# Kernel tuning notes

Measured on AMD Instinct MI355X. Metric: run time of the kernel, lower is better.

The kernel has to match this reference:

```python
import jax, jax.numpy as jnp
import numpy as np

N_NODES, N_GRAPHS, HIDDEN, N_BRANCH = 131072, 4096, 512, 4
G_HEAD, N_HEAD = 50, 3  # graph head dim, node head dim; var_output=1 doubles MLP output


def setup_inputs() -> dict:
    key = jax.random.key(0)
    ks = jax.random.split(key, 10)
    s = 0.02
    x = jax.random.normal(ks[0], (N_NODES, HIDDEN), dtype=jnp.float32)
    # sorted graph assignment: 32 nodes per graph (consecutive, as unique_consecutive assumes)
    batch = (jnp.arange(N_NODES) // (N_NODES // N_GRAPHS)).astype(jnp.int32)
    dataset_ids = jax.random.randint(ks[1], (N_GRAPHS,), 0, N_BRANCH).astype(jnp.int32)
    return {
        "x": x,
        "Ws": jax.random.normal(ks[2], (N_BRANCH, HIDDEN, HIDDEN)) * s,
        "bs": jnp.zeros((N_BRANCH, HIDDEN)),
        "Wg": jax.random.normal(ks[3], (N_BRANCH, HIDDEN, 2 * G_HEAD)) * s,
        "bg": jnp.zeros((N_BRANCH, 2 * G_HEAD)),
        "Wn1": jax.random.normal(ks[4], (N_BRANCH, HIDDEN, HIDDEN)) * s,
        "bn1": jnp.zeros((N_BRANCH, HIDDEN)),
        "Wn2": jax.random.normal(ks[5], (N_BRANCH, HIDDEN, 2 * N_HEAD)) * s,
        "bn2": jnp.zeros((N_BRANCH, 2 * N_HEAD)),
        "batch": batch,
        "dataset_ids": dataset_ids,
    }


def reference(x, Ws, bs, Wg, bg, Wn1, bn1, Wn2, bn2, batch, dataset_ids):
    n_graphs = dataset_ids.shape[0]
    n_branch = Ws.shape[0]
    ghd = Wg.shape[2] // 2
    nhd = Wn2.shape[2] // 2
    # mean pooling per graph (graph_pool_fn with 'mean' reduction)
    ones = jnp.ones((x.shape[0],), dtype=x.dtype)
    counts = jax.ops.segment_sum(ones, batch, num_segments=n_graphs)
    x_graph = jax.ops.segment_sum(x, batch, num_segments=n_graphs) / counts[:, None]
    node_ds = dataset_ids[batch]  # per-node branch id (repeat_interleave of graph mask)

    g_head = jnp.zeros((n_graphs, ghd), dtype=x.dtype)
    g_var = jnp.zeros((n_graphs, ghd), dtype=x.dtype)
    n_head_out = jnp.zeros((x.shape[0], nhd), dtype=x.dtype)
    n_var = jnp.zeros((x.shape[0], nhd), dtype=x.dtype)
    for b in range(n_branch):  # fixed small branch set (structurally distinct experts)
        # graph head branch: graph_shared MLP -> head MLP, scatter back via mask
        hg = jax.nn.relu(x_graph @ Ws[b] + bs[b])
        og = hg @ Wg[b] + bg[b]
        mg = (dataset_ids == b).astype(x.dtype)[:, None]
        g_head = g_head + mg * og[:, :ghd]
        g_var = g_var + mg * (og[:, ghd:] ** 2)
        # node head branch (node_NN_type == 'mlp')
        hn = jax.nn.relu(x @ Wn1[b] + bn1[b])
        on = hn @ Wn2[b] + bn2[b]
        mn = (node_ds == b).astype(x.dtype)[:, None]
        n_head_out = n_head_out + mn * on[:, :nhd]
        n_var = n_var + mn * (on[:, nhd:] ** 2)
    return (g_head, g_var, n_head_out, n_var)
```

## Files before the change

### kernel.cpp

```cpp
#include <hip/hip_runtime.h>

#define N_NODES  131072
#define N_GRAPHS 4096
#define HID      512

typedef float  f32x4  __attribute__((ext_vector_type(4)));
typedef __bf16 bf16x8 __attribute__((ext_vector_type(8)));
typedef unsigned short u16x8 __attribute__((ext_vector_type(8)));

__device__ __forceinline__ unsigned short f2bf(float f) {
  unsigned int u = __builtin_bit_cast(unsigned int, f);
  u += 0x7FFFu + ((u >> 16) & 1u);
  return (unsigned short)(u >> 16);
}
__device__ __forceinline__ f32x4 mfma_bf16(bf16x8 a, bf16x8 b, f32x4 c) {
  return __builtin_amdgcn_mfma_f32_16x16x32_bf16(a, b, c, 0, 0, 0);
}

__global__ __launch_bounds__(256) void bucket_kernel(
    const int* __restrict__ dsid, int* __restrict__ perm, int* __restrict__ meta) {
  __shared__ int cnt[4], base[4], off[4];
  int t = threadIdx.x;
  if (t < 4) { cnt[t] = 0; off[t] = 0; }
  __syncthreads();
  for (int g = t; g < N_GRAPHS; g += 256) atomicAdd(&cnt[dsid[g]], 1);
  __syncthreads();
  if (t == 0) {
    int s = 0;
    for (int b = 0; b < 4; ++b) { base[b] = s; s += cnt[b]; meta[b] = cnt[b]; }
  }
  __syncthreads();
  for (int g = t; g < N_GRAPHS; g += 256) {
    int b = dsid[g];
    int p = base[b] + atomicAdd(&off[b], 1);
    perm[p] = g;
  }
}

__global__ __launch_bounds__(256) void prep_wf_kernel(
    const float* __restrict__ Wn1, const float* __restrict__ Ws,
    unsigned short* __restrict__ W1Tf, unsigned short* __restrict__ WsTf) {
  __shared__ unsigned short lt[8192];
  const int bid = blockIdx.x;
  const int which = bid >> 7;
  const int b  = (bid >> 5) & 3;
  const int hf = bid & 31;
  const float* src = (which ? Ws : Wn1) + (size_t)b * 512 * 512 + hf * 16;
  unsigned short* dst = (which ? WsTf : W1Tf) + (size_t)(b * 32 + hf) * 8192;
  const int t = threadIdx.x;
  for (int i = t; i < 8192; i += 256) {
    int k = i >> 4;
    int n = i & 15;
    float v = src[(size_t)k * 512 + n];
    int kk = k >> 5, lane = n + ((k >> 3) & 3) * 16, e = k & 7;
    lt[(kk * 64 + lane) * 8 + e] = f2bf(v);
  }
  __syncthreads();
  u16x8* d8 = (u16x8*)dst;
  const u16x8* s8 = (const u16x8*)lt;
  for (int i = t; i < 1024; i += 256) d8[i] = s8[i];
}

__global__ __launch_bounds__(256) void prep_wg_kernel(
    const float* __restrict__ Wg, unsigned short* __restrict__ WgT) {
  int idx = blockIdx.x * 256 + threadIdx.x;
  int b = idx >> 16;
  int r = (idx >> 9) & 127;
  int k = idx & 511;
  float v = (r < 100) ? Wg[(b * 512 + k) * 100 + r] : 0.f;
  WgT[idx] = f2bf(v);
}

#define NT_MAX 2050
__global__ __launch_bounds__(1024, 2) void node_kernel(
    const float* __restrict__ x,
    const int* __restrict__ meta,
    const int* __restrict__ perm,
    const unsigned short* __restrict__ W1Tf,
    const float* __restrict__ bn1,
    const float* __restrict__ Wn2,
    const float* __restrict__ bn2,
    unsigned short* __restrict__ xg,
    float* __restrict__ n_head,
    float* __restrict__ n_var) {
  __shared__ __align__(16) unsigned short xfrag[2][8192];
  __shared__ __align__(16) float psum[2][16][128];

  const int4 cvv = *(const int4*)meta;
  const int cnts[4] = {cvv.x, cvv.y, cvv.z, cvv.w};
  int i = blockIdx.x, branch = -1, permOff = 0, nvalid = 0, pb = 0;
  for (int b = 0; b < 4; ++b) {
    int nt = (cnts[b] + 1) >> 1;
    if (branch < 0 && i < nt) { branch = b; permOff = pb + i * 2; nvalid = min(2, cnts[b] - i * 2); }
    if (branch < 0) i -= nt;
    pb += cnts[b];
  }
  if (branch < 0) return;

  const int t    = threadIdx.x;
  const int lane = t & 63;
  const int w    = t >> 6;
  const int l15  = lane & 15;
  const int l4   = lane >> 4;

  const int g0 = perm[permOff];
  const int g1 = perm[permOff + (nvalid > 1 ? 1 : 0)];

  const int sr = t >> 4;
  const int so = t & 15;
  const float* srcbase = x + ((size_t)(sr >= 32 ? g1 : g0) * 32 + (sr & 31)) * HID + so * 8;
  const int sn = sr >> 4, sl15 = sr & 15, skkl = so >> 2, sl4 = so & 3;
  const int welem = ((sn * 4 + skkl) * 64 + ((sl4 << 4) | (sl15 ^ so))) * 8;

  const unsigned short* wb0 = W1Tf + (size_t)(branch * 32 + w * 2) * 8192 + lane * 8;

  f32x4 acc[2][4];
  #pragma unroll
  for (int m = 0; m < 2; ++m)
    #pragma unroll
    for (int n = 0; n < 4; ++n) acc[m][n] = (f32x4)0.f;

  float4 p0 = *(const float4*)(srcbase);
  float4 p1 = *(const float4*)(srcbase + 4);

  #pragma unroll
  for (int c = 0; c < 4; ++c) {
    u16x8 ua;
    ua[0]=f2bf(p0.x); ua[1]=f2bf(p0.y); ua[2]=f2bf(p0.z); ua[3]=f2bf(p0.w);
    ua[4]=f2bf(p1.x); ua[5]=f2bf(p1.y); ua[6]=f2bf(p1.z); ua[7]=f2bf(p1.w);
    *(u16x8*)&xfrag[c & 1][welem] = ua;

    float s[8];
    s[0]=p0.x; s[1]=p0.y; s[2]=p0.z; s[3]=p0.w;
    s[4]=p1.x; s[5]=p1.y; s[6]=p1.z; s[7]=p1.w;
    #pragma unroll
    for (int j = 0; j < 8; ++j) {
      s[j] += __shfl_xor(s[j], 16);
      s[j] += __shfl_xor(s[j], 32);
    }
    if (lane < 16) {
      f32x4 a4; a4[0]=s[0]; a4[1]=s[1]; a4[2]=s[2]; a4[3]=s[3];
      f32x4 b4; b4[0]=s[4]; b4[1]=s[5]; b4[2]=s[6]; b4[3]=s[7];
      *(f32x4*)&psum[c & 1][w][lane * 8]     = a4;
      *(f32x4*)&psum[c & 1][w][lane * 8 + 4] = b4;
    }

    if (c < 3) {
      p0 = *(const float4*)(srcbase + (c + 1) * 128);
      p1 = *(const float4*)(srcbase + (c + 1) * 128 + 4);
    }
    __syncthreads();

    if (t < 256) {
      int gg = t >> 7, cc = t & 127;
      if (gg == 0 || nvalid > 1) {
        float sv = 0.f;
        #pragma unroll
        for (int j = 0; j < 8; ++j) sv += psum[c & 1][gg * 8 + j][cc];
        xg[(size_t)(gg ? g1 : g0) * HID + c * 128 + cc] = f2bf(sv * (1.f / 32.f));
      }
    }

    __builtin_amdgcn_s_setprio(1);
    #pragma unroll
    for (int kk = 0; kk < 4; ++kk) {
      bf16x8 af0 = *(const bf16x8*)(wb0 + (size_t)(c * 4 + kk) * 512);
      bf16x8 af1 = *(const bf16x8*)(wb0 + 8192 + (size_t)(c * 4 + kk) * 512);
      const int rslot = (l4 << 4) | (l15 ^ (kk * 4 + l4));
      bf16x8 bfr[4];
      #pragma unroll
      for (int n = 0; n < 4; ++n)
        bfr[n] = *(const bf16x8*)&xfrag[c & 1][((n * 4 + kk) * 64 + rslot) * 8];
      #pragma unroll
      for (int n = 0; n < 4; ++n) {
        acc[0][n] = mfma_bf16(af0, bfr[n], acc[0][n]);
        acc[1][n] = mfma_bf16(af1, bfr[n], acc[1][n]);
      }
    }
    __builtin_amdgcn_s_setprio(0);
  }

  __syncthreads();

  float part[4][6];
  #pragma unroll
  for (int n = 0; n < 4; ++n)
    #pragma unroll
    for (int j = 0; j < 6; ++j) part[n][j] = 0.f;
  const float* W2 = Wn2 + branch * HID * 6;
  const float* B1 = bn1 + branch * HID;
  #pragma unroll
  for (int m = 0; m < 2; ++m) {
    #pragma unroll
    for (int r = 0; r < 4; ++r) {
      int hcol = w * 32 + m * 16 + l4 * 4 + r;
      float b1 = B1[hcol];
      float w2[6];
      #pragma unroll
      for (int j = 0; j < 6; ++j) w2[j] = W2[hcol * 6 + j];
      #pragma unroll
      for (int n = 0; n < 4; ++n) {
        float h = fmaxf(acc[m][n][r] + b1, 0.f);
        #pragma unroll
        for (int j = 0; j < 6; ++j) part[n][j] += h * w2[j];
      }
    }
  }
  #pragma unroll
  for (int n = 0; n < 4; ++n)
    #pragma unroll
    for (int j = 0; j < 6; ++j) {
      part[n][j] += __shfl_xor(part[n][j], 16);
      part[n][j] += __shfl_xor(part[n][j], 32);
    }
  float (*red)[17][7] = (float (*)[17][7])&xfrag[0][0];
  if (lane < 16) {
    #pragma unroll
    for (int n = 0; n < 4; ++n)
      #pragma unroll
      for (int j = 0; j < 6; ++j) red[n * 16 + l15][w][j] = part[n][j];
  }
  __syncthreads();
  if (t < 64) {
    int row = t;
    if (row < nvalid * 32) {
      int node = (row < 32 ? g0 : g1) * 32 + (row & 31);
      #pragma unroll
      for (int j = 0; j < 6; ++j) {
        float sv = bn2[branch * 6 + j];
        #pragma unroll
        for (int ww = 0; ww < 16; ++ww) sv += red[row][ww][j];
        if (j < 3) n_head[(size_t)node * 3 + j] = sv;
        else       n_var[(size_t)node * 3 + (j - 3)] = sv * sv;
      }
    }
  }
}

#define GT_MAX 67
__global__ __launch_bounds__(512, 4) void gstage1_kernel(
    const unsigned short* __restrict__ xg,
    const int* __restrict__ meta,
    const int* __restrict__ perm,
    const unsigned short* __restrict__ WsTf,
    const float* __restrict__ bs_,
    unsigned short* __restrict__ hg) {
  __shared__ __align__(16) unsigned short xtile[4 * 16 * 512];
  __shared__ int gidl[64];

  const int4 cv = *(const int4*)meta;
  const int cnts[4] = {cv.x, cv.y, cv.z, cv.w};

  int i = blockIdx.x, branch = -1, permOff = 0, nvalid = 0, pb = 0;
  for (int b = 0; b < 4; ++b) {
    int gt = (cnts[b] + 63) >> 6;
    if (branch < 0 && i < gt) { branch = b; permOff = pb + i * 64; nvalid = min(64, cnts[b] - i * 64); }
    if (branch < 0) i -= gt;
    pb += cnts[b];
  }
  if (branch < 0) return;

  const int t    = threadIdx.x;
  const int lane = t & 63;
  const int w    = t >> 6;
  const int l15  = lane & 15;
  const int l4   = lane >> 4;

  if (t < 64) gidl[t] = perm[permOff + min(t, nvalid - 1)];
  __syncthreads();

  for (int idx = t; idx < 4096; idx += 512) {
    int row = idx >> 6;
    int c8  = (idx & 63) * 8;
    u16x8 v = *(const u16x8*)&xg[(size_t)gidl[row] * HID + c8];
    int kk = c8 >> 5, ln = (c8 >> 3) & 3;
    *(u16x8*)&xtile[(((row >> 4) * 16 + kk) * 64 + ((row & 15) + ln * 16)) * 8] = v;
  }
  __syncthreads();

  f32x4 acc[4][4];
  #pragma unroll
  for (int m = 0; m < 4; ++m)
    #pragma unroll
    for (int n = 0; n < 4; ++n) acc[m][n] = (f32x4)0.f;

  const unsigned short* wbase = WsTf + ((size_t)(branch * 32 + w * 4)) * 8192 + lane * 8;
  const unsigned short* xbase = xtile + lane * 8;
  #pragma unroll
  for (int kk = 0; kk < 16; ++kk) {
    bf16x8 af[4];
    #pragma unroll
    for (int m = 0; m < 4; ++m)
      af[m] = *(const bf16x8*)(wbase + (m * 16 + kk) * 512);
    bf16x8 bfr[4];
    #pragma unroll
    for (int n = 0; n < 4; ++n)
      bfr[n] = *(const bf16x8*)(xbase + (n * 16 + kk) * 512);
    #pragma unroll
    for (int m = 0; m < 4; ++m)
      #pragma unroll
      for (int n = 0; n < 4; ++n)
        acc[m][n] = mfma_bf16(af[m], bfr[n], acc[m][n]);
  }

  const float* B1 = bs_ + branch * HID;
  #pragma unroll
  for (int m = 0; m < 4; ++m) {
    #pragma unroll
    for (int n = 0; n < 4; ++n) {
      int row = n * 16 + l15;
      if (row < nvalid) {
        int g = gidl[row];
        int hcb = w * 64 + m * 16 + l4 * 4;
        ushort4 hv;
        hv.x = f2bf(fmaxf(acc[m][n][0] + B1[hcb + 0], 0.f));
        hv.y = f2bf(fmaxf(acc[m][n][1] + B1[hcb + 1], 0.f));
        hv.z = f2bf(fmaxf(acc[m][n][2] + B1[hcb + 2], 0.f));
        hv.w = f2bf(fmaxf(acc[m][n][3] + B1[hcb + 3], 0.f));
        *(ushort4*)(hg + (size_t)g * HID + hcb) = hv;
      }
    }
  }
}

#define G2_MAX 259
__global__ __launch_bounds__(256) void gstage2_kernel(
    const int* __restrict__ meta,
    const int* __restrict__ perm,
    const unsigned short* __restrict__ hg,
    const unsigned short* __restrict__ WgT,
    const float* __restrict__ bg,
    float* __restrict__ g_head,
    float* __restrict__ g_var) {
  __shared__ int gidl[16];
  const int4 cv = *(const int4*)meta;
  const int cnts[4] = {cv.x, cv.y, cv.z, cv.w};

  int i = blockIdx.x, branch = -1, permOff = 0, nvalid = 0, pb = 0;
  for (int b = 0; b < 4; ++b) {
    int gt = (cnts[b] + 15) >> 4;
    if (branch < 0 && i < gt) { branch = b; permOff = pb + i * 16; nvalid = min(16, cnts[b] - i * 16); }
    if (branch < 0) i -= gt;
    pb += cnts[b];
  }
  if (branch < 0) return;

  const int t    = threadIdx.x;
  const int lane = t & 63;
  const int w    = t >> 6;
  const int l15  = lane & 15;
  const int l4   = lane >> 4;

  if (t < 16) gidl[t] = perm[permOff + min(t, nvalid - 1)];
  __syncthreads();

  f32x4 acc2[2];
  acc2[0] = (f32x4)0.f; acc2[1] = (f32x4)0.f;
  const unsigned short* arow = hg + (size_t)gidl[l15] * HID + l4 * 8;
  const unsigned short* brow = WgT + ((size_t)branch * 128 + w * 32 + l15) * 512 + l4 * 8;
  #pragma unroll
  for (int ks = 0; ks < 16; ++ks) {
    bf16x8 a  = *(const bf16x8*)(arow + ks * 32);
    bf16x8 b0 = *(const bf16x8*)(brow + ks * 32);
    bf16x8 b1 = *(const bf16x8*)(brow + 16 * 512 + ks * 32);
    acc2[0] = mfma_bf16(a, b0, acc2[0]);
    acc2[1] = mfma_bf16(a, b1, acc2[1]);
  }
  #pragma unroll
  for (int n2 = 0; n2 < 2; ++n2) {
    int j = w * 32 + n2 * 16 + l15;
    if (j < 100) {
      float bias = bg[branch * 100 + j];
      #pragma unroll
      for (int rr = 0; rr < 4; ++rr) {
        int r = l4 * 4 + rr;
        if (r < nvalid) {
          int g = gidl[r];
          float val = acc2[n2][rr] + bias;
          if (j < 50) g_head[(size_t)g * 50 + j] = val;
          else        g_var[(size_t)g * 50 + (j - 50)] = val * val;
        }
      }
    }
  }
}

extern "C" void kernel_launch(void* const* d_in, const int* in_sizes, int n_in,
                              void* d_out, int out_size, void* d_ws, size_t ws_size,
                              hipStream_t stream) {
  const float* x    = (const float*)d_in[0];
  const float* Ws   = (const float*)d_in[1];
  const float* bs   = (const float*)d_in[2];
  const float* Wg   = (const float*)d_in[3];
  const float* bg   = (const float*)d_in[4];
  const float* Wn1  = (const float*)d_in[5];
  const float* bn1  = (const float*)d_in[6];
  const float* Wn2  = (const float*)d_in[7];
  const float* bn2  = (const float*)d_in[8];
  const int* dsid   = (const int*)d_in[10];

  float* out    = (float*)d_out;
  float* g_head = out;
  float* g_var  = out + (size_t)N_GRAPHS * 50;
  float* n_head = out + (size_t)2 * N_GRAPHS * 50;
  float* n_var  = n_head + (size_t)N_NODES * 3;

  char* ws = (char*)d_ws;
  int* perm = (int*)(ws);
  int* meta = (int*)(ws + 16384);
  unsigned short* W1Tf = (unsigned short*)(ws + 16640);
  unsigned short* WsTf = (unsigned short*)(ws + 2113792);
  unsigned short* WgT  = (unsigned short*)(ws + 4210944);
  unsigned short* xg   = (unsigned short*)(ws + 4735232);
  unsigned short* hg   = (unsigned short*)(ws + 8929536);
  if (ws_size < 13123840) return;

  bucket_kernel<<<dim3(1), dim3(256), 0, stream>>>(dsid, perm, meta);
  prep_wf_kernel<<<dim3(256), dim3(256), 0, stream>>>(Wn1, Ws, W1Tf, WsTf);
  prep_wg_kernel<<<dim3(1024), dim3(256), 0, stream>>>(Wg, WgT);
  node_kernel<<<dim3(NT_MAX), dim3(1024), 0, stream>>>(
      x, meta, perm, W1Tf, bn1, Wn2, bn2, xg, n_head, n_var);
  gstage1_kernel<<<dim3(GT_MAX), dim3(512), 0, stream>>>(
      xg, meta, perm, WsTf, bs, hg);
  gstage2_kernel<<<dim3(G2_MAX), dim3(256), 0, stream>>>(
      meta, perm, hg, WgT, bg, g_head, g_var);
}
```

Measured before the change: 220.6 us.

## Restructure node kernel to one graph per 256-thread block

The node MLP kernel now processes one graph (32 nodes) per 256-thread block, reading the branch directly from dataset_ids instead of the bucketed permutation. Each wave covers 128 hidden columns over 8 K-chunks, which gives more MFMA work per B fragment and a smaller shared-memory footprint so more blocks fit per CU. Each block now streams the full branch weight matrix for only 32 nodes instead of 64, which doubles the weight traffic from L2 relative to node data. The mean-pool reduction is deferred until after the matmul loop.

```diff
diff --git a/kernel.cpp b/kernel.cpp
--- a/kernel.cpp
+++ b/kernel.cpp
@@ -71,11 +71,9 @@
   WgT[idx] = f2bf(v);
 }
 
-#define NT_MAX 2050
-__global__ __launch_bounds__(1024, 2) void node_kernel(
+__global__ __launch_bounds__(256, 4) void node_kernel(
     const float* __restrict__ x,
-    const int* __restrict__ meta,
-    const int* __restrict__ perm,
+    const int* __restrict__ dsid,
     const unsigned short* __restrict__ W1Tf,
     const float* __restrict__ bn1,
     const float* __restrict__ Wn2,
@@ -83,48 +81,35 @@
     unsigned short* __restrict__ xg,
     float* __restrict__ n_head,
     float* __restrict__ n_var) {
-  __shared__ __align__(16) unsigned short xfrag[2][8192];
-  __shared__ __align__(16) float psum[2][16][128];
-
-  const int4 cvv = *(const int4*)meta;
-  const int cnts[4] = {cvv.x, cvv.y, cvv.z, cvv.w};
-  int i = blockIdx.x, branch = -1, permOff = 0, nvalid = 0, pb = 0;
-  for (int b = 0; b < 4; ++b) {
-    int nt = (cnts[b] + 1) >> 1;
-    if (branch < 0 && i < nt) { branch = b; permOff = pb + i * 2; nvalid = min(2, cnts[b] - i * 2); }
-    if (branch < 0) i -= nt;
-    pb += cnts[b];
-  }
-  if (branch < 0) return;
-
+  __shared__ __align__(16) unsigned short xfrag[2][2048];
+  __shared__ __align__(16) float psum[8][4][64];
+  __shared__ __align__(16) float red[4][32][6];
+
+  const int g = blockIdx.x;
+  const int b = dsid[g];
   const int t    = threadIdx.x;
   const int lane = t & 63;
   const int w    = t >> 6;
   const int l15  = lane & 15;
   const int l4   = lane >> 4;
 
-  const int g0 = perm[permOff];
-  const int g1 = perm[permOff + (nvalid > 1 ? 1 : 0)];
-
-  const int sr = t >> 4;
-  const int so = t & 15;
-  const float* srcbase = x + ((size_t)(sr >= 32 ? g1 : g0) * 32 + (sr & 31)) * HID + so * 8;
-  const int sn = sr >> 4, sl15 = sr & 15, skkl = so >> 2, sl4 = so & 3;
-  const int welem = ((sn * 4 + skkl) * 64 + ((sl4 << 4) | (sl15 ^ so))) * 8;
-
-  const unsigned short* wb0 = W1Tf + (size_t)(branch * 32 + w * 2) * 8192 + lane * 8;
-
-  f32x4 acc[2][4];
-  #pragma unroll
-  for (int m = 0; m < 2; ++m)
-    #pragma unroll
-    for (int n = 0; n < 4; ++n) acc[m][n] = (f32x4)0.f;
-
-  float4 p0 = *(const float4*)(srcbase);
-  float4 p1 = *(const float4*)(srcbase + 4);
-
-  #pragma unroll
-  for (int c = 0; c < 4; ++c) {
+  const int srow = t >> 3;
+  const int oct  = t & 7;
+  const float* src = x + ((size_t)g * 32 + srow) * HID + oct * 8;
+  const int sn = srow >> 4, skk = oct >> 2, sl4 = oct & 3;
+  const int welem = ((sn * 2 + skk) * 64 + ((sl4 << 4) | ((srow & 15) ^ oct))) * 8;
+
+  const unsigned short* wb = W1Tf + (size_t)(b * 32 + w * 8) * 8192 + lane * 8;
+
+  f32x4 acc[8][2];
+  #pragma unroll
+  for (int m = 0; m < 8; ++m) { acc[m][0] = (f32x4)0.f; acc[m][1] = (f32x4)0.f; }
+
+  float4 p0 = *(const float4*)(src);
+  float4 p1 = *(const float4*)(src + 4);
+
+  #pragma unroll
+  for (int c = 0; c < 8; ++c) {
     u16x8 ua;
     ua[0]=f2bf(p0.x); ua[1]=f2bf(p0.y); ua[2]=f2bf(p0.z); ua[3]=f2bf(p0.w);
     ua[4]=f2bf(p1.x); ua[5]=f2bf(p1.y); ua[6]=f2bf(p1.z); ua[7]=f2bf(p1.w);
@@ -135,71 +120,66 @@
     s[4]=p1.x; s[5]=p1.y; s[6]=p1.z; s[7]=p1.w;
     #pragma unroll
     for (int j = 0; j < 8; ++j) {
+      s[j] += __shfl_xor(s[j], 8);
       s[j] += __shfl_xor(s[j], 16);
       s[j] += __shfl_xor(s[j], 32);
     }
-    if (lane < 16) {
+    if (lane < 8) {
       f32x4 a4; a4[0]=s[0]; a4[1]=s[1]; a4[2]=s[2]; a4[3]=s[3];
       f32x4 b4; b4[0]=s[4]; b4[1]=s[5]; b4[2]=s[6]; b4[3]=s[7];
-      *(f32x4*)&psum[c & 1][w][lane * 8]     = a4;
-      *(f32x4*)&psum[c & 1][w][lane * 8 + 4] = b4;
-    }
-
-    if (c < 3) {
-      p0 = *(const float4*)(srcbase + (c + 1) * 128);
-      p1 = *(const float4*)(srcbase + (c + 1) * 128 + 4);
+      *(f32x4*)&psum[c][w][lane * 8]     = a4;
+      *(f32x4*)&psum[c][w][lane * 8 + 4] = b4;
+    }
+
+    if (c < 7) {
+      p0 = *(const float4*)(src + (c + 1) * 64);
+      p1 = *(const float4*)(src + (c + 1) * 64 + 4);
     }
     __syncthreads();
 
-    if (t < 256) {
-      int gg = t >> 7, cc = t & 127;
-      if (gg == 0 || nvalid > 1) {
-        float sv = 0.f;
-        #pragma unroll
-        for (int j = 0; j < 8; ++j) sv += psum[c & 1][gg * 8 + j][cc];
-        xg[(size_t)(gg ? g1 : g0) * HID + c * 128 + cc] = f2bf(sv * (1.f / 32.f));
+    __builtin_amdgcn_s_setprio(1);
+    #pragma unroll
+    for (int kk = 0; kk < 2; ++kk) {
+      const int kkG = c * 2 + kk;
+      const int rslot = (l4 << 4) | (l15 ^ (kk * 4 + l4));
+      bf16x8 bfr0 = *(const bf16x8*)&xfrag[c & 1][((kk) * 64 + rslot) * 8];
+      bf16x8 bfr1 = *(const bf16x8*)&xfrag[c & 1][((2 + kk) * 64 + rslot) * 8];
+      #pragma unroll
+      for (int m = 0; m < 8; ++m) {
+        bf16x8 af = *(const bf16x8*)(wb + (size_t)m * 8192 + kkG * 512);
+        acc[m][0] = mfma_bf16(af, bfr0, acc[m][0]);
+        acc[m][1] = mfma_bf16(af, bfr1, acc[m][1]);
       }
     }
-
-    __builtin_amdgcn_s_setprio(1);
-    #pragma unroll
-    for (int kk = 0; kk < 4; ++kk) {
-      bf16x8 af0 = *(const bf16x8*)(wb0 + (size_t)(c * 4 + kk) * 512);
-      bf16x8 af1 = *(const bf16x8*)(wb0 + 8192 + (size_t)(c * 4 + kk) * 512);
-      const int rslot = (l4 << 4) | (l15 ^ (kk * 4 + l4));
-      bf16x8 bfr[4];
-      #pragma unroll
-      for (int n = 0; n < 4; ++n)
-        bfr[n] = *(const bf16x8*)&xfrag[c & 1][((n * 4 + kk) * 64 + rslot) * 8];
-      #pragma unroll
-      for (int n = 0; n < 4; ++n) {
-        acc[0][n] = mfma_bf16(af0, bfr[n], acc[0][n]);
-        acc[1][n] = mfma_bf16(af1, bfr[n], acc[1][n]);
-      }
-    }
     __builtin_amdgcn_s_setprio(0);
   }
 
-  __syncthreads();
-
-  float part[4][6];
-  #pragma unroll
-  for (int n = 0; n < 4; ++n)
+  #pragma unroll
+  for (int h = 0; h < 2; ++h) {
+    int col = t + h * 256;
+    int c = col >> 6, cc = col & 63;
+    float sv = psum[c][0][cc] + psum[c][1][cc] + psum[c][2][cc] + psum[c][3][cc];
+    xg[(size_t)g * HID + col] = f2bf(sv * (1.f / 32.f));
+  }
+
+  float part[2][6];
+  #pragma unroll
+  for (int n = 0; n < 2; ++n)
     #pragma unroll
     for (int j = 0; j < 6; ++j) part[n][j] = 0.f;
-  const float* W2 = Wn2 + branch * HID * 6;
-  const float* B1 = bn1 + branch * HID;
-  #pragma unroll
-  for (int m = 0; m < 2; ++m) {
+  const float* W2 = Wn2 + b * HID * 6;
+  const float* B1 = bn1 + b * HID;
+  #pragma unroll
+  for (int m = 0; m < 8; ++m) {
     #pragma unroll
     for (int r = 0; r < 4; ++r) {
-      int hcol = w * 32 + m * 16 + l4 * 4 + r;
+      int hcol = w * 128 + m * 16 + l4 * 4 + r;
       float b1 = B1[hcol];
       float w2[6];
       #pragma unroll
       for (int j = 0; j < 6; ++j) w2[j] = W2[hcol * 6 + j];
       #pragma unroll
-      for (int n = 0; n < 4; ++n) {
+      for (int n = 0; n < 2; ++n) {
         float h = fmaxf(acc[m][n][r] + b1, 0.f);
         #pragma unroll
         for (int j = 0; j < 6; ++j) part[n][j] += h * w2[j];
@@ -207,32 +187,28 @@
     }
   }
   #pragma unroll
-  for (int n = 0; n < 4; ++n)
+  for (int n = 0; n < 2; ++n)
     #pragma unroll
     for (int j = 0; j < 6; ++j) {
       part[n][j] += __shfl_xor(part[n][j], 16);
       part[n][j] += __shfl_xor(part[n][j], 32);
     }
-  float (*red)[17][7] = (float (*)[17][7])&xfrag[0][0];
   if (lane < 16) {
     #pragma unroll
-    for (int n = 0; n < 4; ++n)
-      #pragma unroll
-      for (int j = 0; j < 6; ++j) red[n * 16 + l15][w][j] = part[n][j];
-  }
-  __syncthreads();
-  if (t < 64) {
+    for (int n = 0; n < 2; ++n)
+      #pragma unroll
+      for (int j = 0; j < 6; ++j) red[w][n * 16 + l15][j] = part[n][j];
+  }
+  __syncthreads();
+  if (t < 32) {
     int row = t;
-    if (row < nvalid * 32) {
-      int node = (row < 32 ? g0 : g1) * 32 + (row & 31);
-      #pragma unroll
-      for (int j = 0; j < 6; ++j) {
-        float sv = bn2[branch * 6 + j];
-        #pragma unroll
-        for (int ww = 0; ww < 16; ++ww) sv += red[row][ww][j];
-        if (j < 3) n_head[(size_t)node * 3 + j] = sv;
-        else       n_var[(size_t)node * 3 + (j - 3)] = sv * sv;
-      }
+    int node = g * 32 + row;
+    #pragma unroll
+    for (int j = 0; j < 6; ++j) {
+      float sv = red[0][row][j] + red[1][row][j] + red[2][row][j] + red[3][row][j]
+               + bn2[b * 6 + j];
+      if (j < 3) n_head[(size_t)node * 3 + j] = sv;
+      else       n_var[(size_t)node * 3 + (j - 3)] = sv * sv;
     }
   }
 }
@@ -418,8 +394,8 @@
   bucket_kernel<<<dim3(1), dim3(256), 0, stream>>>(dsid, perm, meta);
   prep_wf_kernel<<<dim3(256), dim3(256), 0, stream>>>(Wn1, Ws, W1Tf, WsTf);
   prep_wg_kernel<<<dim3(1024), dim3(256), 0, stream>>>(Wg, WgT);
-  node_kernel<<<dim3(NT_MAX), dim3(1024), 0, stream>>>(
-      x, meta, perm, W1Tf, bn1, Wn2, bn2, xg, n_head, n_var);
+  node_kernel<<<dim3(N_GRAPHS), dim3(256), 0, stream>>>(
+      x, dsid, W1Tf, bn1, Wn2, bn2, xg, n_head, n_var);
   gstage1_kernel<<<dim3(GT_MAX), dim3(512), 0, stream>>>(
       xg, meta, perm, WsTf, bs, hg);
   gstage2_kernel<<<dim3(G2_MAX), dim3(256), 0, stream>>>(
```

New measurement: 393.4 us. +78.4%, slower.

## Split node stage into chunked bf16 convert/pool and GEMM kernels

Applied to the files above, without the earlier changes.

The fused node kernel is replaced by a per-chunk pair of kernels. A convert_pool kernel writes x as bf16 MFMA-fragment tiles plus pooled graph means, and a node_gemm kernel with 512 threads loads two graphs' full tiles into shared memory and runs the whole K loop from LDS. Graph bucketing is now done per 1024-graph chunk so each GEMM launch only touches data converted for its chunk, which should keep it L2-resident. This adds a large bf16 workspace round trip, 8 launches instead of 1, and extra partially filled blocks in the graph stages.

```diff
diff --git a/kernel.cpp b/kernel.cpp
--- a/kernel.cpp
+++ b/kernel.cpp
@@ -3,6 +3,9 @@
 #define N_NODES  131072
 #define N_GRAPHS 4096
 #define HID      512
+#define CHUNK_G  1024
+#define N_CHUNKS 4
+#define B_BLOCKS 516
 
 typedef float  f32x4  __attribute__((ext_vector_type(4)));
 typedef __bf16 bf16x8 __attribute__((ext_vector_type(8)));
@@ -17,23 +20,22 @@
   return __builtin_amdgcn_mfma_f32_16x16x32_bf16(a, b, c, 0, 0, 0);
 }
 
-__global__ __launch_bounds__(256) void bucket_kernel(
+__global__ __launch_bounds__(512) void bucket_kernel(
     const int* __restrict__ dsid, int* __restrict__ perm, int* __restrict__ meta) {
-  __shared__ int cnt[4], base[4], off[4];
+  __shared__ int cnt[N_CHUNKS][4], base[N_CHUNKS][4], off[N_CHUNKS][4];
   int t = threadIdx.x;
-  if (t < 4) { cnt[t] = 0; off[t] = 0; }
-  __syncthreads();
-  for (int g = t; g < N_GRAPHS; g += 256) atomicAdd(&cnt[dsid[g]], 1);
-  __syncthreads();
-  if (t == 0) {
+  if (t < N_CHUNKS * 4) { (&cnt[0][0])[t] = 0; (&off[0][0])[t] = 0; }
+  __syncthreads();
+  for (int g = t; g < N_GRAPHS; g += 512) atomicAdd(&cnt[g / CHUNK_G][dsid[g]], 1);
+  __syncthreads();
+  if (t < N_CHUNKS) {
     int s = 0;
-    for (int b = 0; b < 4; ++b) { base[b] = s; s += cnt[b]; meta[b] = cnt[b]; }
-  }
-  __syncthreads();
-  for (int g = t; g < N_GRAPHS; g += 256) {
-    int b = dsid[g];
-    int p = base[b] + atomicAdd(&off[b], 1);
-    perm[p] = g;
+    for (int b = 0; b < 4; ++b) { base[t][b] = s; s += cnt[t][b]; meta[t * 4 + b] = cnt[t][b]; }
+  }
+  __syncthreads();
+  for (int g = t; g < N_GRAPHS; g += 512) {
+    int c = g / CHUNK_G, b = dsid[g];
+    perm[c * CHUNK_G + base[c][b] + atomicAdd(&off[c][b], 1)] = g;
   }
 }
 
@@ -71,22 +73,71 @@
   WgT[idx] = f2bf(v);
 }
 
-#define NT_MAX 2050
-__global__ __launch_bounds__(1024, 2) void node_kernel(
+__global__ __launch_bounds__(512) void convert_pool_kernel(
     const float* __restrict__ x,
-    const int* __restrict__ meta,
-    const int* __restrict__ perm,
+    unsigned short* __restrict__ xb,
+    unsigned short* __restrict__ xg,
+    int gbase) {
+  const int gl = blockIdx.x;
+  const int g  = gbase + gl;
+  const int t = threadIdx.x;
+  const int lane = t & 63, w = t >> 6, l15 = lane & 15, l4 = lane >> 4;
+  const float* xs = x + (size_t)g * 32 * HID;
+  unsigned short* xd = xb + (size_t)gl * 16384;
+  float ps[2][8];
+  #pragma unroll
+  for (int j = 0; j < 2; ++j)
+    #pragma unroll
+    for (int e = 0; e < 8; ++e) ps[j][e] = 0.f;
+  #pragma unroll
+  for (int i = 0; i < 4; ++i) {
+    const int kk = w * 2 + (i & 1), nf = i >> 1, pi = i & 1;
+    const int row = nf * 16 + l15, col = kk * 32 + l4 * 8;
+    float4 p0 = *(const float4*)(xs + (size_t)row * HID + col);
+    float4 p1 = *(const float4*)(xs + (size_t)row * HID + col + 4);
+    u16x8 ua;
+    ua[0]=f2bf(p0.x); ua[1]=f2bf(p0.y); ua[2]=f2bf(p0.z); ua[3]=f2bf(p0.w);
+    ua[4]=f2bf(p1.x); ua[5]=f2bf(p1.y); ua[6]=f2bf(p1.z); ua[7]=f2bf(p1.w);
+    *(u16x8*)&xd[((nf * 16 + kk) * 64 + lane) * 8] = ua;
+    ps[pi][0]+=p0.x; ps[pi][1]+=p0.y; ps[pi][2]+=p0.z; ps[pi][3]+=p0.w;
+    ps[pi][4]+=p1.x; ps[pi][5]+=p1.y; ps[pi][6]+=p1.z; ps[pi][7]+=p1.w;
+  }
+  #pragma unroll
+  for (int j = 0; j < 2; ++j)
+    #pragma unroll
+    for (int e = 0; e < 8; ++e) {
+      ps[j][e] += __shfl_xor(ps[j][e], 1);
+      ps[j][e] += __shfl_xor(ps[j][e], 2);
+      ps[j][e] += __shfl_xor(ps[j][e], 4);
+      ps[j][e] += __shfl_xor(ps[j][e], 8);
+    }
+  if (l15 == 0) {
+    #pragma unroll
+    for (int j = 0; j < 2; ++j) {
+      int kk = w * 2 + j;
+      u16x8 o;
+      #pragma unroll
+      for (int e = 0; e < 8; ++e) o[e] = f2bf(ps[j][e] * (1.f / 32.f));
+      *(u16x8*)&xg[(size_t)g * HID + kk * 32 + l4 * 8] = o;
+    }
+  }
+}
+
+__global__ __launch_bounds__(512, 4) void node_gemm_kernel(
+    const unsigned short* __restrict__ xb,
+    const int* __restrict__ metac,
+    const int* __restrict__ permc,
     const unsigned short* __restrict__ W1Tf,
     const float* __restrict__ bn1,
     const float* __restrict__ Wn2,
     const float* __restrict__ bn2,
-    unsigned short* __restrict__ xg,
     float* __restrict__ n_head,
-    float* __restrict__ n_var) {
-  __shared__ __align__(16) unsigned short xfrag[2][8192];
-  __shared__ __align__(16) float psum[2][16][128];
-
-  const int4 cvv = *(const int4*)meta;
+    float* __restrict__ n_var,
+    int gbase) {
+  __shared__ __align__(16) unsigned short xtile[32768];
+  __shared__ __align__(16) float red[8][64][6];
+
+  const int4 cvv = *(const int4*)metac;
   const int cnts[4] = {cvv.x, cvv.y, cvv.z, cvv.w};
   int i = blockIdx.x, branch = -1, permOff = 0, nvalid = 0, pb = 0;
   for (int b = 0; b < 4; ++b) {
@@ -97,115 +148,72 @@
   }
   if (branch < 0) return;
 
-  const int t    = threadIdx.x;
-  const int lane = t & 63;
-  const int w    = t >> 6;
-  const int l15  = lane & 15;
-  const int l4   = lane >> 4;
-
-  const int g0 = perm[permOff];
-  const int g1 = perm[permOff + (nvalid > 1 ? 1 : 0)];
-
-  const int sr = t >> 4;
-  const int so = t & 15;
-  const float* srcbase = x + ((size_t)(sr >= 32 ? g1 : g0) * 32 + (sr & 31)) * HID + so * 8;
-  const int sn = sr >> 4, sl15 = sr & 15, skkl = so >> 2, sl4 = so & 3;
-  const int welem = ((sn * 4 + skkl) * 64 + ((sl4 << 4) | (sl15 ^ so))) * 8;
-
-  const unsigned short* wb0 = W1Tf + (size_t)(branch * 32 + w * 2) * 8192 + lane * 8;
-
-  f32x4 acc[2][4];
-  #pragma unroll
-  for (int m = 0; m < 2; ++m)
-    #pragma unroll
-    for (int n = 0; n < 4; ++n) acc[m][n] = (f32x4)0.f;
-
-  float4 p0 = *(const float4*)(srcbase);
-  float4 p1 = *(const float4*)(srcbase + 4);
-
-  #pragma unroll
-  for (int c = 0; c < 4; ++c) {
-    u16x8 ua;
-    ua[0]=f2bf(p0.x); ua[1]=f2bf(p0.y); ua[2]=f2bf(p0.z); ua[3]=f2bf(p0.w);
-    ua[4]=f2bf(p1.x); ua[5]=f2bf(p1.y); ua[6]=f2bf(p1.z); ua[7]=f2bf(p1.w);
-    *(u16x8*)&xfrag[c & 1][welem] = ua;
-
-    float s[8];
-    s[0]=p0.x; s[1]=p0.y; s[2]=p0.z; s[3]=p0.w;
-    s[4]=p1.x; s[5]=p1.y; s[6]=p1.z; s[7]=p1.w;
-    #pragma unroll
-    for (int j = 0; j < 8; ++j) {
-      s[j] += __shfl_xor(s[j], 16);
-      s[j] += __shfl_xor(s[j], 32);
-    }
-    if (lane < 16) {
-      f32x4 a4; a4[0]=s[0]; a4[1]=s[1]; a4[2]=s[2]; a4[3]=s[3];
-      f32x4 b4; b4[0]=s[4]; b4[1]=s[5]; b4[2]=s[6]; b4[3]=s[7];
-      *(f32x4*)&psum[c & 1][w][lane * 8]     = a4;
-      *(f32x4*)&psum[c & 1][w][lane * 8 + 4] = b4;
-    }
-
-    if (c < 3) {
-      p0 = *(const float4*)(srcbase + (c + 1) * 128);
-      p1 = *(const float4*)(srcbase + (c + 1) * 128 + 4);
-    }
-    __syncthreads();
-
-    if (t < 256) {
-      int gg = t >> 7, cc = t & 127;
-      if (gg == 0 || nvalid > 1) {
-        float sv = 0.f;
-        #pragma unroll
-        for (int j = 0; j < 8; ++j) sv += psum[c & 1][gg * 8 + j][cc];
-        xg[(size_t)(gg ? g1 : g0) * HID + c * 128 + cc] = f2bf(sv * (1.f / 32.f));
-      }
-    }
-
-    __builtin_amdgcn_s_setprio(1);
-    #pragma unroll
-    for (int kk = 0; kk < 4; ++kk) {
-      bf16x8 af0 = *(const bf16x8*)(wb0 + (size_t)(c * 4 + kk) * 512);
-      bf16x8 af1 = *(const bf16x8*)(wb0 + 8192 + (size_t)(c * 4 + kk) * 512);
-      const int rslot = (l4 << 4) | (l15 ^ (kk * 4 + l4));
+  const int t = threadIdx.x;
+  const int lane = t & 63, w = t >> 6, l15 = lane & 15, l4 = lane >> 4;
+  const int g0 = permc[permOff];
+  const int g1 = permc[permOff + (nvalid > 1 ? 1 : 0)];
+
+  const unsigned short* s0 = xb + (size_t)(g0 - gbase) * 16384;
+  const unsigned short* s1 = xb + (size_t)(g1 - gbase) * 16384;
+  #pragma unroll
+  for (int ii = 0; ii < 4; ++ii) {
+    int idx = (t + ii * 512) * 8;
+    *(u16x8*)&xtile[idx]         = *(const u16x8*)&s0[idx];
+    *(u16x8*)&xtile[16384 + idx] = *(const u16x8*)&s1[idx];
+  }
+  __syncthreads();
+
+  float part[4][6];
+  #pragma unroll
+  for (int n = 0; n < 4; ++n)
+    #pragma unroll
+    for (int j = 0; j < 6; ++j) part[n][j] = 0.f;
+  const float* B1 = bn1 + branch * HID;
+  const float* W2 = Wn2 + branch * HID * 6;
+
+  #pragma unroll
+  for (int s = 0; s < 2; ++s) {
+    const unsigned short* wb =
+        W1Tf + ((size_t)(branch * 32 + s * 16 + w * 2)) * 8192 + lane * 8;
+    f32x4 acc[2][4];
+    #pragma unroll
+    for (int m = 0; m < 2; ++m)
+      #pragma unroll
+      for (int n = 0; n < 4; ++n) acc[m][n] = (f32x4)0.f;
+
+    #pragma unroll
+    for (int kk = 0; kk < 16; ++kk) {
+      bf16x8 af0 = *(const bf16x8*)(wb + kk * 512);
+      bf16x8 af1 = *(const bf16x8*)(wb + 8192 + kk * 512);
       bf16x8 bfr[4];
       #pragma unroll
       for (int n = 0; n < 4; ++n)
-        bfr[n] = *(const bf16x8*)&xfrag[c & 1][((n * 4 + kk) * 64 + rslot) * 8];
+        bfr[n] = *(const bf16x8*)&xtile[(n * 16 + kk) * 512 + lane * 8];
       #pragma unroll
       for (int n = 0; n < 4; ++n) {
         acc[0][n] = mfma_bf16(af0, bfr[n], acc[0][n]);
         acc[1][n] = mfma_bf16(af1, bfr[n], acc[1][n]);
       }
     }
-    __builtin_amdgcn_s_setprio(0);
-  }
-
-  __syncthreads();
-
-  float part[4][6];
-  #pragma unroll
-  for (int n = 0; n < 4; ++n)
-    #pragma unroll
-    for (int j = 0; j < 6; ++j) part[n][j] = 0.f;
-  const float* W2 = Wn2 + branch * HID * 6;
-  const float* B1 = bn1 + branch * HID;
-  #pragma unroll
-  for (int m = 0; m < 2; ++m) {
-    #pragma unroll
-    for (int r = 0; r < 4; ++r) {
-      int hcol = w * 32 + m * 16 + l4 * 4 + r;
-      float b1 = B1[hcol];
-      float w2[6];
-      #pragma unroll
-      for (int j = 0; j < 6; ++j) w2[j] = W2[hcol * 6 + j];
-      #pragma unroll
-      for (int n = 0; n < 4; ++n) {
-        float h = fmaxf(acc[m][n][r] + b1, 0.f);
+    #pragma unroll
+    for (int m = 0; m < 2; ++m) {
+      #pragma unroll
+      for (int r = 0; r < 4; ++r) {
+        int hcol = (s * 16 + w * 2 + m) * 16 + l4 * 4 + r;
+        float b1 = B1[hcol];
+        float w2[6];
         #pragma unroll
-        for (int j = 0; j < 6; ++j) part[n][j] += h * w2[j];
+        for (int j = 0; j < 6; ++j) w2[j] = W2[hcol * 6 + j];
+        #pragma unroll
+        for (int n = 0; n < 4; ++n) {
+          float h = fmaxf(acc[m][n][r] + b1, 0.f);
+          #pragma unroll
+          for (int j = 0; j < 6; ++j) part[n][j] += h * w2[j];
+        }
       }
     }
   }
+
   #pragma unroll
   for (int n = 0; n < 4; ++n)
     #pragma unroll
@@ -213,23 +221,22 @@
       part[n][j] += __shfl_xor(part[n][j], 16);
       part[n][j] += __shfl_xor(part[n][j], 32);
     }
-  float (*red)[17][7] = (float (*)[17][7])&xfrag[0][0];
   if (lane < 16) {
     #pragma unroll
     for (int n = 0; n < 4; ++n)
       #pragma unroll
-      for (int j = 0; j < 6; ++j) red[n * 16 + l15][w][j] = part[n][j];
+      for (int j = 0; j < 6; ++j) red[w][n * 16 + l15][j] = part[n][j];
   }
   __syncthreads();
   if (t < 64) {
-    int row = t;
-    if (row < nvalid * 32) {
-      int node = (row < 32 ? g0 : g1) * 32 + (row & 31);
+    int q = t >> 5;
+    if (q < nvalid) {
+      int node = (q ? g1 : g0) * 32 + (t & 31);
       #pragma unroll
       for (int j = 0; j < 6; ++j) {
         float sv = bn2[branch * 6 + j];
         #pragma unroll
-        for (int ww = 0; ww < 16; ++ww) sv += red[row][ww][j];
+        for (int ww = 0; ww < 8; ++ww) sv += red[ww][t][j];
         if (j < 3) n_head[(size_t)node * 3 + j] = sv;
         else       n_var[(size_t)node * 3 + (j - 3)] = sv * sv;
       }
@@ -237,7 +244,7 @@
   }
 }
 
-#define GT_MAX 67
+#define GT_MAX 80
 __global__ __launch_bounds__(512, 4) void gstage1_kernel(
     const unsigned short* __restrict__ xg,
     const int* __restrict__ meta,
@@ -245,26 +252,24 @@
     const unsigned short* __restrict__ WsTf,
     const float* __restrict__ bs_,
     unsigned short* __restrict__ hg) {
-  __shared__ __align__(16) unsigned short xtile[4 * 16 * 512];
+  __shared__ __align__(16) unsigned short xtile[32768];
   __shared__ int gidl[64];
 
-  const int4 cv = *(const int4*)meta;
-  const int cnts[4] = {cv.x, cv.y, cv.z, cv.w};
-
-  int i = blockIdx.x, branch = -1, permOff = 0, nvalid = 0, pb = 0;
-  for (int b = 0; b < 4; ++b) {
-    int gt = (cnts[b] + 63) >> 6;
-    if (branch < 0 && i < gt) { branch = b; permOff = pb + i * 64; nvalid = min(64, cnts[b] - i * 64); }
-    if (branch < 0) i -= gt;
-    pb += cnts[b];
+  int i = blockIdx.x, branch = -1, permOff = 0, nvalid = 0;
+  for (int c = 0; c < N_CHUNKS; ++c) {
+    int pb = 0;
+    for (int b = 0; b < 4; ++b) {
+      int cnt = meta[c * 4 + b];
+      int gt = (cnt + 63) >> 6;
+      if (branch < 0 && i < gt) { branch = b; permOff = c * CHUNK_G + pb + i * 64; nvalid = min(64, cnt - i * 64); }
+      if (branch < 0) i -= gt;
+      pb += cnt;
+    }
   }
   if (branch < 0) return;
 
-  const int t    = threadIdx.x;
-  const int lane = t & 63;
-  const int w    = t >> 6;
-  const int l15  = lane & 15;
-  const int l4   = lane >> 4;
+  const int t = threadIdx.x;
+  const int lane = t & 63, w = t >> 6, l15 = lane & 15, l4 = lane >> 4;
 
   if (t < 64) gidl[t] = perm[permOff + min(t, nvalid - 1)];
   __syncthreads();
@@ -323,7 +328,7 @@
   }
 }
 
-#define G2_MAX 259
+#define G2_MAX 272
 __global__ __launch_bounds__(256) void gstage2_kernel(
     const int* __restrict__ meta,
     const int* __restrict__ perm,
@@ -333,23 +338,21 @@
     float* __restrict__ g_head,
     float* __restrict__ g_var) {
   __shared__ int gidl[16];
-  const int4 cv = *(const int4*)meta;
-  const int cnts[4] = {cv.x, cv.y, cv.z, cv.w};
-
-  int i = blockIdx.x, branch = -1, permOff = 0, nvalid = 0, pb = 0;
-  for (int b = 0; b < 4; ++b) {
-    int gt = (cnts[b] + 15) >> 4;
-    if (branch < 0 && i < gt) { branch = b; permOff = pb + i * 16; nvalid = min(16, cnts[b] - i * 16); }
-    if (branch < 0) i -= gt;
-    pb += cnts[b];
+  int i = blockIdx.x, branch = -1, permOff = 0, nvalid = 0;
+  for (int c = 0; c < N_CHUNKS; ++c) {
+    int pb = 0;
+    for (int b = 0; b < 4; ++b) {
+      int cnt = meta[c * 4 + b];
+      int gt = (cnt + 15) >> 4;
+      if (branch < 0 && i < gt) { branch = b; permOff = c * CHUNK_G + pb + i * 16; nvalid = min(16, cnt - i * 16); }
+      if (branch < 0) i -= gt;
+      pb += cnt;
+    }
   }
   if (branch < 0) return;
 
-  const int t    = threadIdx.x;
-  const int lane = t & 63;
-  const int w    = t >> 6;
-  const int l15  = lane & 15;
-  const int l4   = lane >> 4;
+  const int t = threadIdx.x;
+  const int lane = t & 63, w = t >> 6, l15 = lane & 15, l4 = lane >> 4;
 
   if (t < 16) gidl[t] = perm[permOff + min(t, nvalid - 1)];
   __syncthreads();
@@ -413,13 +416,19 @@
   unsigned short* WgT  = (unsigned short*)(ws + 4210944);
   unsigned short* xg   = (unsigned short*)(ws + 4735232);
   unsigned short* hg   = (unsigned short*)(ws + 8929536);
-  if (ws_size < 13123840) return;
-
-  bucket_kernel<<<dim3(1), dim3(256), 0, stream>>>(dsid, perm, meta);
+  unsigned short* xb   = (unsigned short*)(ws + 13123840);
+  if (ws_size < 46678272) return;
+
+  bucket_kernel<<<dim3(1), dim3(512), 0, stream>>>(dsid, perm, meta);
   prep_wf_kernel<<<dim3(256), dim3(256), 0, stream>>>(Wn1, Ws, W1Tf, WsTf);
   prep_wg_kernel<<<dim3(1024), dim3(256), 0, stream>>>(Wg, WgT);
-  node_kernel<<<dim3(NT_MAX), dim3(1024), 0, stream>>>(
-      x, meta, perm, W1Tf, bn1, Wn2, bn2, xg, n_head, n_var);
+  for (int c = 0; c < N_CHUNKS; ++c) {
+    convert_pool_kernel<<<dim3(CHUNK_G), dim3(512), 0, stream>>>(
+        x, xb, xg, c * CHUNK_G);
+    node_gemm_kernel<<<dim3(B_BLOCKS), dim3(512), 0, stream>>>(
+        xb, meta + c * 4, perm + c * CHUNK_G, W1Tf, bn1, Wn2, bn2,
+        n_head, n_var, c * CHUNK_G);
+  }
   gstage1_kernel<<<dim3(GT_MAX), dim3(512), 0, stream>>>(
       xg, meta, perm, WsTf, bs, hg);
   gstage2_kernel<<<dim3(G2_MAX), dim3(256), 0, stream>>>(
```

After: 726.3 us. +229.3%, slower.
